# Kernel tuning notes

Hardware: AMD Instinct MI355X
Metric: run time of the kernel (lower is better)

The kernel has to match this reference:

```python
import jax, jax.numpy as jnp
import numpy as np

N_NODES = 50000
N_EDGES = 800000
HIDDEN = 128
N_LAYERS = 3
N_MASKED = 25000
N_GRAPHS = 64


def setup_inputs() -> dict:
    key = jax.random.key(0)
    ks = jax.random.split(key, 8)
    scale = 1.0 / np.sqrt(HIDDEN)
    return {
        "x": jax.random.normal(ks[0], (N_NODES, HIDDEN), dtype=jnp.float32),
        "edge_index": jax.random.randint(ks[1], (2, N_EDGES), 0, N_NODES, dtype=jnp.int64),
        "mask": jax.random.randint(ks[2], (N_MASKED,), 0, N_NODES, dtype=jnp.int64),
        "batch": jnp.sort(jax.random.randint(ks[3], (N_MASKED,), 0, N_GRAPHS, dtype=jnp.int64)),
        "conv_w": jax.random.normal(ks[4], (N_LAYERS, HIDDEN, HIDDEN), dtype=jnp.float32) * scale,
        "conv_b": jnp.zeros((N_LAYERS, HIDDEN), dtype=jnp.float32),
        "lt1_w": jax.random.normal(ks[5], (HIDDEN,), dtype=jnp.float32) * scale,
        "lt1_b": jnp.zeros((1,), dtype=jnp.float32),
    }


def reference(x, edge_index, mask, batch, conv_w, conv_b, lt1_w, lt1_b):
    n = x.shape[0]
    # GCNConv: add self-loops, symmetric normalization D^-1/2 (A+I) D^-1/2
    loops = jnp.arange(n, dtype=edge_index.dtype)
    src = jnp.concatenate([edge_index[0], loops])
    dst = jnp.concatenate([edge_index[1], loops])
    deg = jax.ops.segment_sum(jnp.ones_like(src, dtype=x.dtype), dst, num_segments=n)
    dinv = jax.lax.rsqrt(deg)  # deg >= 1 because of self-loops
    norm = (dinv[src] * dinv[dst])[:, None]  # [E+N, 1]

    h = x
    for l in range(N_LAYERS):
        hw = h @ conv_w[l]                                  # [N, H]
        agg = jax.ops.segment_sum(hw[src] * norm, dst, num_segments=n)
        h = jax.nn.elu(agg + conv_b[l])                     # dropout is identity in eval mode

    xm = h[mask]                                            # [M, H] masked-node features
    pooled = jax.ops.segment_max(xm, batch, num_segments=N_GRAPHS)  # global_max_pool
    return pooled @ lt1_w[:, None] + lt1_b                  # [G, 1]
```

## Files before the change

### kernel.cpp

```cpp
#include <hip/hip_runtime.h>
#include <math.h>

#define N_NODES  50000
#define N_EDGES  800000
#define HIDDEN   128
#define N_LAYERS 3
#define N_MASKED 25000
#define N_GRAPHS 64
#define XSLICE   6250
#define EPB      8192
#define NCHUNK   ((N_EDGES + EPB - 1) / EPB)

typedef __attribute__((ext_vector_type(8))) short bf16x8;
typedef __attribute__((ext_vector_type(4))) float f32x4;

#define GLOAD_LDS16(g, l) \
    __builtin_amdgcn_global_load_lds((const __attribute__((address_space(1))) void*)(g), \
                                     (__attribute__((address_space(3))) void*)(l), 16, 0, 0)

__device__ __forceinline__ unsigned fmap(float f) {
    unsigned u = __float_as_uint(f);
    return (u & 0x80000000u) ? ~u : (u | 0x80000000u);
}
__device__ __forceinline__ float funmap(unsigned u) {
    return __uint_as_float((u & 0x80000000u) ? (u & 0x7FFFFFFFu) : ~u);
}

__device__ __forceinline__ unsigned pack_split(float x) {
    unsigned u = __float_as_uint(x);
    unsigned hi = (u + 0x7fffu + ((u >> 16) & 1u)) >> 16;
    float rem = x - __uint_as_float(hi << 16);
    unsigned v = __float_as_uint(rem);
    unsigned lo = (v + 0x7fffu + ((v >> 16) & 1u)) >> 16;
    return hi | (lo << 16);
}

__global__ void init_kernel(unsigned* __restrict__ deg, unsigned* __restrict__ gmax,
                            const float* __restrict__ W,
                            unsigned short* __restrict__ Whi,
                            unsigned short* __restrict__ Wlo) {
    const int b = blockIdx.x;
    if (b < 196) {
        int i = b * 256 + threadIdx.x;
        if (i < N_NODES) deg[i] = 0u;
    } else if (b < 228) {
        int i = (b - 196) * 256 + threadIdx.x;
        if (i < N_GRAPHS * 128) gmax[i] = 0x007FFFFFu;
    } else {
        int idx = (b - 228) * 256 + threadIdx.x;
        if (idx < 3 * 16384) {
            int j     = idx & 7;
            int lane  = (idx >> 3) & 63;
            int ct    = (idx >> 9) & 7;
            int ks    = (idx >> 12) & 3;
            int layer = idx >> 14;
            int k = ks * 32 + (lane >> 4) * 8 + j;
            int n = ct * 16 + (lane & 15);
            unsigned p = pack_split(W[layer * 16384 + k * 128 + n]);
            Whi[idx] = (unsigned short)(p & 0xffffu);
            Wlo[idx] = (unsigned short)(p >> 16);
        }
    }
}

__global__ void xpack_kernel(const float* __restrict__ x, unsigned* __restrict__ xp, int n) {
    int i = blockIdx.x * 256 + threadIdx.x;
    if (i < n) xp[i] = pack_split(x[i]);
}

__global__ void count_deg_kernel(const int* __restrict__ dst, unsigned* __restrict__ deg) {
    const int xcd = blockIdx.x & 7;
    const int chunk = blockIdx.x >> 3;
    const int lo = xcd * XSLICE, hi = lo + XSLICE;
    const int base = chunk * EPB;
    const int end = (base + EPB < N_EDGES) ? base + EPB : N_EDGES;
    for (int e = base + threadIdx.x * 4; e < end; e += 256 * 4) {
        int4 d4 = *(const int4*)(dst + e);
        if (d4.x >= lo && d4.x < hi) atomicAdd(&deg[d4.x], 1u);
        if (d4.y >= lo && d4.y < hi) atomicAdd(&deg[d4.y], 1u);
        if (d4.z >= lo && d4.z < hi) atomicAdd(&deg[d4.z], 1u);
        if (d4.w >= lo && d4.w < hi) atomicAdd(&deg[d4.w], 1u);
    }
}

__global__ void scan_block_kernel(const unsigned* __restrict__ deg, unsigned* __restrict__ incl,
                                  unsigned* __restrict__ bsum) {
    __shared__ unsigned s[1024];
    int i = blockIdx.x * 1024 + threadIdx.x;
    unsigned v = (i < N_NODES) ? deg[i] : 0u;
    s[threadIdx.x] = v;
    __syncthreads();
    for (int off = 1; off < 1024; off <<= 1) {
        unsigned t = (threadIdx.x >= off) ? s[threadIdx.x - off] : 0u;
        __syncthreads();
        s[threadIdx.x] += t;
        __syncthreads();
    }
    if (i < N_NODES) incl[i] = s[threadIdx.x];
    if (threadIdx.x == 1023) bsum[blockIdx.x] = s[1023];
}

__global__ void scan_bsum_kernel(unsigned* __restrict__ bsum, int n) {
    int lane = threadIdx.x;
    unsigned v = (lane < n) ? bsum[lane] : 0u;
    #pragma unroll
    for (int off = 1; off < 64; off <<= 1) {
        unsigned t = __shfl_up(v, off);
        if (lane >= off) v += t;
    }
    unsigned ex = __shfl_up(v, 1);
    if (lane == 0) ex = 0u;
    if (lane < n) bsum[lane] = ex;
}

__global__ void scan_finalize_kernel(const unsigned* __restrict__ incl,
                                     const unsigned* __restrict__ bsum_ex,
                                     const unsigned* __restrict__ deg,
                                     unsigned* __restrict__ row_ptr,
                                     unsigned* __restrict__ cursor,
                                     float* __restrict__ dinv) {
    int i = blockIdx.x * blockDim.x + threadIdx.x;
    if (i <= N_NODES) {
        unsigned v = (i == 0) ? 0u : incl[i - 1] + bsum_ex[(i - 1) >> 10];
        row_ptr[i] = v;
        if (i < N_NODES) {
            cursor[(size_t)i << 4] = v;
            dinv[i] = rsqrtf((float)(deg[i] + 1u));
        }
    }
}

__global__ void fill_csr_kernel(const int* __restrict__ src, const int* __restrict__ dst,
                                unsigned* __restrict__ cursor, int* __restrict__ csr_src) {
    const int xcd = blockIdx.x & 7;
    const int chunk = blockIdx.x >> 3;
    const int lo = xcd * XSLICE, hi = lo + XSLICE;
    const int base = chunk * EPB;
    const int end = (base + EPB < N_EDGES) ? base + EPB : N_EDGES;
    for (int e = base + threadIdx.x * 4; e < end; e += 256 * 4) {
        int4 d4 = *(const int4*)(dst + e);
        int4 s4 = *(const int4*)(src + e);
        if (d4.x >= lo && d4.x < hi) csr_src[atomicAdd(&cursor[(size_t)d4.x << 4], 1u)] = s4.x;
        if (d4.y >= lo && d4.y < hi) csr_src[atomicAdd(&cursor[(size_t)d4.y << 4], 1u)] = s4.y;
        if (d4.z >= lo && d4.z < hi) csr_src[atomicAdd(&cursor[(size_t)d4.z << 4], 1u)] = s4.z;
        if (d4.w >= lo && d4.w < hi) csr_src[atomicAdd(&cursor[(size_t)d4.w << 4], 1u)] = s4.w;
    }
}

template<int MODE>
__global__ __launch_bounds__(512, 1) void mfma_gemm_kernel(const unsigned* __restrict__ Ap,
                                                           const unsigned short* __restrict__ Wh,
                                                           const unsigned short* __restrict__ Wl,
                                                           const float* __restrict__ dinv,
                                                           const float* __restrict__ bias,
                                                           const int* __restrict__ batch,
                                                           unsigned* __restrict__ gmax,
                                                           float* __restrict__ Out,
                                                           int nrows) {
    extern __shared__ char smem[];
    unsigned short* WhL = (unsigned short*)smem;
    unsigned short* WlL = (unsigned short*)(smem + 32768);
    uint4* AL4 = (uint4*)(smem + 65536);
    const int tid = threadIdx.x;
    const int lane = tid & 63;
    const int w = tid >> 6;

    #pragma unroll
    for (int i = 0; i < 4; ++i) {
        int m = tid + i * 512;
        GLOAD_LDS16((const char*)Wh + (size_t)m * 16, smem + (size_t)m * 16);
        GLOAD_LDS16((const char*)Wl + (size_t)m * 16, smem + 32768 + (size_t)m * 16);
    }

    const int ntiles = (nrows + 127) >> 7;
    const int rloc = w * 16 + (lane & 15);
    const int rx = rloc & 7;
    const int colBase = lane & 15;
    const int rgrp = lane >> 4;

    for (int t = blockIdx.x; t < ntiles; t += gridDim.x) {
        const int tileBase = t * 128;
        __syncthreads();

        #pragma unroll
        for (int i = 0; i < 8; ++i) {
            int n = tid + i * 512;
            int r = n >> 5;
            int c = n & 31;
            int grow = tileBase + r;
            if (grow > nrows - 1) grow = nrows - 1;
            GLOAD_LDS16(Ap + (size_t)grow * 128 + ((c ^ (r & 7)) << 2),
                        smem + 65536 + (size_t)n * 16);
        }
        __syncthreads();

        f32x4 acc[8];
        #pragma unroll
        for (int c = 0; c < 8; ++c) acc[c] = (f32x4){0.f, 0.f, 0.f, 0.f};

        #pragma unroll
        for (int ks = 0; ks < 4; ++ks) {
            int c0 = ks * 8 + (lane >> 4) * 2;
            uint4 a0 = AL4[rloc * 32 + (c0 ^ rx)];
            uint4 a1 = AL4[rloc * 32 + ((c0 + 1) ^ rx)];
            unsigned pv[8] = {a0.x, a0.y, a0.z, a0.w, a1.x, a1.y, a1.z, a1.w};
            bf16x8 ah, al;
            #pragma unroll
            for (int j = 0; j < 8; ++j) {
                ah[j] = (short)(pv[j] & 0xffffu);
                al[j] = (short)(pv[j] >> 16);
            }
            const unsigned short* wbh = WhL + ks * 4096 + lane * 8;
            const unsigned short* wbl = WlL + ks * 4096 + lane * 8;
            #pragma unroll
            for (int ct = 0; ct < 8; ++ct) {
                bf16x8 bh = *(const bf16x8*)(wbh + ct * 512);
                bf16x8 bl = *(const bf16x8*)(wbl + ct * 512);
                acc[ct] = __builtin_amdgcn_mfma_f32_16x16x32_bf16(ah, bh, acc[ct], 0, 0, 0);
                acc[ct] = __builtin_amdgcn_mfma_f32_16x16x32_bf16(al, bh, acc[ct], 0, 0, 0);
                acc[ct] = __builtin_amdgcn_mfma_f32_16x16x32_bf16(ah, bl, acc[ct], 0, 0, 0);
            }
        }

        #pragma unroll
        for (int r = 0; r < 4; ++r) {
            int row = tileBase + w * 16 + rgrp * 4 + r;
            if (row >= nrows) continue;
            float d = 0.f;
            int bofs = 0;
            if (MODE == 0 || MODE == 1) d = dinv[row];
            if (MODE == 2) bofs = batch[row] * 128;
            #pragma unroll
            for (int ct = 0; ct < 8; ++ct) {
                int col = ct * 16 + colBase;
                float o = acc[ct][r];
                if (MODE == 0) {
                    Out[(size_t)row * 128 + col] = o * d;
                } else {
                    o += bias[col];
                    o = o > 0.f ? o : expm1f(o);
                    if (MODE == 1) Out[(size_t)row * 128 + col] = o * d;
                    else           atomicMax(&gmax[bofs + col], fmap(o));
                }
            }
        }
    }
}

template<int GMODE>
__global__ __launch_bounds__(256) void gather_kernel(const float* __restrict__ tab,
                                                     const unsigned* __restrict__ row_ptr,
                                                     const int* __restrict__ csr_src,
                                                     const float* __restrict__ dinv,
                                                     const float* __restrict__ bias,
                                                     float* __restrict__ outf,
                                                     unsigned* __restrict__ outp,
                                                     const int* __restrict__ nodes,
                                                     int n_items) {
    int wid = (blockIdx.x * blockDim.x + threadIdx.x) >> 6;
    int w = wid >> 1;
    if (w >= n_items) return;
    const int f = ((wid & 1) << 6) | (threadIdx.x & 63);
    const int v = nodes ? nodes[w] : w;

    const unsigned s0 = row_ptr[v], e0 = row_ptr[v + 1];
    const float* __restrict__ base = tab + f;

    float acc[8];
    #pragma unroll
    for (int j = 0; j < 8; ++j) acc[j] = 0.f;
    acc[0] = base[(size_t)v << 7];

    unsigned i = s0;
    if (i + 8 <= e0) {
        int idx[8];
        #pragma unroll
        for (int j = 0; j < 8; ++j) idx[j] = csr_src[i + j];
        for (; i + 16 <= e0; i += 8) {
            int nxt[8];
            #pragma unroll
            for (int j = 0; j < 8; ++j) nxt[j] = csr_src[i + 8 + j];
            #pragma unroll
            for (int j = 0; j < 8; ++j) acc[j] += base[(size_t)idx[j] << 7];
            #pragma unroll
            for (int j = 0; j < 8; ++j) idx[j] = nxt[j];
        }
        #pragma unroll
        for (int j = 0; j < 8; ++j) acc[j] += base[(size_t)idx[j] << 7];
        i += 8;
    }
    if (i + 4 <= e0) {
        #pragma unroll
        for (int j = 0; j < 4; ++j) acc[j] += base[(size_t)csr_src[i + j] << 7];
        i += 4;
    }
    for (; i < e0; ++i) acc[0] += base[(size_t)csr_src[i] << 7];

    float dv = dinv[v];
    float sumall = ((acc[0] + acc[1]) + (acc[2] + acc[3])) +
                   ((acc[4] + acc[5]) + (acc[6] + acc[7]));
    if (GMODE == 0) {
        float o = dv * sumall + bias[f];
        o = o > 0.f ? o : expm1f(o);
        outf[((size_t)w << 7) + f] = o * dv;
    } else {
        outp[((size_t)w << 7) + f] = pack_split(dv * sumall);
    }
}

__global__ void pool_finish_kernel(const unsigned* __restrict__ gmax,
                                   const float* __restrict__ w, const float* __restrict__ b,
                                   float* __restrict__ out) {
    const int g = blockIdx.x;
    const int f = threadIdx.x;
    float val = funmap(gmax[g * 128 + f]) * w[f];
    #pragma unroll
    for (int off = 32; off > 0; off >>= 1) val += __shfl_down(val, off);
    __shared__ float ps[2];
    if ((threadIdx.x & 63) == 0) ps[threadIdx.x >> 6] = val;
    __syncthreads();
    if (threadIdx.x == 0) out[g] = ps[0] + ps[1] + b[0];
}

extern "C" void kernel_launch(void* const* d_in, const int* in_sizes, int n_in,
                              void* d_out, int out_size, void* d_ws, size_t ws_size,
                              hipStream_t stream) {
    const float* x      = (const float*)d_in[0];
    const int*   ei     = (const int*)d_in[1];
    const int*   mask   = (const int*)d_in[2];
    const int*   batch  = (const int*)d_in[3];
    const float* conv_w = (const float*)d_in[4];
    const float* conv_b = (const float*)d_in[5];
    const float* lt1_w  = (const float*)d_in[6];
    const float* lt1_b  = (const float*)d_in[7];
    float* out = (float*)d_out;

    const int* e_src = ei;
    const int* e_dst = ei + N_EDGES;

    char* ws = (char*)d_ws;
    auto carve = [&](size_t bytes) { char* p = ws; ws += (bytes + 255) & ~(size_t)255; return p; };
    unsigned* deg     = (unsigned*)carve(N_NODES * 4);
    float*    dinv    = (float*)   carve(N_NODES * 4);
    unsigned* row_ptr = (unsigned*)carve((N_NODES + 1) * 4);
    unsigned* cursor  = (unsigned*)carve((size_t)N_NODES * 64);
    unsigned* bsum    = (unsigned*)carve(64 * 4);
    unsigned* gmax    = (unsigned*)carve(N_GRAPHS * 128 * 4);
    unsigned short* wph = (unsigned short*)carve(3 * 16384 * 2);
    unsigned short* wpl = (unsigned short*)carve(3 * 16384 * 2);
    int*      csr_src = (int*)     carve((size_t)N_EDGES * 4);
    unsigned* xp      = (unsigned*)carve((size_t)N_NODES * HIDDEN * 4);
    char*     reg1    = carve((size_t)N_NODES * HIDDEN * 4);
    char*     reg2    = carve((size_t)N_NODES * HIDDEN * 4);
    unsigned* incl    = (unsigned*)csr_src;

    float*    bufB  = (float*)reg1;
    float*    bufB2 = (float*)reg1;
    float*    bufA  = (float*)reg2;
    unsigned* bufAp = (unsigned*)reg2;
    unsigned* bufCp = (unsigned*)reg2;

    const int NB_SCAN = (N_NODES + 1023) / 1024;

    init_kernel<<<420, 256, 0, stream>>>(deg, gmax, conv_w, wph, wpl);
    xpack_kernel<<<(N_NODES * HIDDEN + 255) / 256, 256, 0, stream>>>(x, xp, N_NODES * HIDDEN);
    count_deg_kernel<<<8 * NCHUNK, 256, 0, stream>>>(e_dst, deg);
    scan_block_kernel<<<NB_SCAN, 1024, 0, stream>>>(deg, incl, bsum);
    scan_bsum_kernel<<<1, 64, 0, stream>>>(bsum, NB_SCAN);
    scan_finalize_kernel<<<(N_NODES + 256) / 256, 256, 0, stream>>>(incl, bsum, deg,
                                                                    row_ptr, cursor, dinv);
    fill_csr_kernel<<<8 * NCHUNK, 256, 0, stream>>>(e_src, e_dst, cursor, csr_src);

    const size_t LDS_BYTES = 131072;
    auto gemm_grid = [](int rows) { int t = (rows + 127) / 128; return t < 256 ? t : 256; };
    auto ga_blocks = [](int items) { return (items * 2 * 64 + 255) / 256; };

    mfma_gemm_kernel<0><<<gemm_grid(N_NODES), 512, LDS_BYTES, stream>>>(
        xp, wph, wpl, dinv, nullptr, nullptr, nullptr, bufA, N_NODES);
    gather_kernel<0><<<ga_blocks(N_NODES), 256, 0, stream>>>(
        bufA, row_ptr, csr_src, dinv, conv_b, bufB, nullptr, nullptr, N_NODES);
    gather_kernel<1><<<ga_blocks(N_NODES), 256, 0, stream>>>(
        bufB, row_ptr, csr_src, dinv, nullptr, nullptr, bufAp, nullptr, N_NODES);
    mfma_gemm_kernel<1><<<gemm_grid(N_NODES), 512, LDS_BYTES, stream>>>(
        bufAp, wph + 16384, wpl + 16384, dinv, conv_b + HIDDEN, nullptr, nullptr,
        bufB2, N_NODES);
    gather_kernel<1><<<ga_blocks(N_MASKED), 256, 0, stream>>>(
        bufB2, row_ptr, csr_src, dinv, nullptr, nullptr, bufCp, mask, N_MASKED);
    mfma_gemm_kernel<2><<<gemm_grid(N_MASKED), 512, LDS_BYTES, stream>>>(
        bufCp, wph + 32768, wpl + 32768, nullptr, conv_b + 2 * HIDDEN, batch, gmax,
        nullptr, N_MASKED);

    pool_finish_kernel<<<N_GRAPHS, HIDDEN, 0, stream>>>(gmax, lt1_w, lt1_b, out);
}
```

Baseline: 362.1 us.

## Build CSR with per-group LDS histograms and cursors instead of global atomics

Degree counting now uses LDS histograms per (edge group, node slice) block and writes partial counts. The scan kernel sums them, and the finalize step turns them into per-group start offsets. The CSR fill then uses LDS cursors instead of global atomics on padded cursor slots. Deg zeroing, weight packing, gmax init and a vectorized x packing are folded into one launch, which removes kernel launches and global atomic traffic. The cost is a 32x N_NODES partial array and a 32-iteration serial loop per node in finalize. Fill parallelism also drops to 256 blocks.

```diff
diff --git a/kernel.cpp b/kernel.cpp
--- a/kernel.cpp
+++ b/kernel.cpp
@@ -8,8 +8,8 @@
 #define N_MASKED 25000
 #define N_GRAPHS 64
 #define XSLICE   6250
-#define EPB      8192
-#define NCHUNK   ((N_EDGES + EPB - 1) / EPB)
+#define NGRP     32
+#define CPG      (N_EDGES / NGRP)
 
 typedef __attribute__((ext_vector_type(8))) short bf16x8;
 typedef __attribute__((ext_vector_type(4))) float f32x4;
@@ -35,19 +35,37 @@
     return hi | (lo << 16);
 }
 
-__global__ void init_kernel(unsigned* __restrict__ deg, unsigned* __restrict__ gmax,
-                            const float* __restrict__ W,
-                            unsigned short* __restrict__ Whi,
-                            unsigned short* __restrict__ Wlo) {
+__global__ void build_kernel(const int* __restrict__ dst, unsigned* __restrict__ partial,
+                             unsigned* __restrict__ gmax, const float* __restrict__ W,
+                             unsigned short* __restrict__ Whi, unsigned short* __restrict__ Wlo,
+                             const float* __restrict__ x, unsigned* __restrict__ xp) {
     const int b = blockIdx.x;
-    if (b < 196) {
-        int i = b * 256 + threadIdx.x;
-        if (i < N_NODES) deg[i] = 0u;
-    } else if (b < 228) {
-        int i = (b - 196) * 256 + threadIdx.x;
+    const int tid = threadIdx.x;
+    if (b < 256) {
+        __shared__ unsigned hist[XSLICE];
+        const int xcd = b & 7;
+        const int g = b >> 3;
+        const int lo = xcd * XSLICE;
+        for (int i = tid; i < XSLICE; i += 256) hist[i] = 0u;
+        __syncthreads();
+        const int base = g * CPG;
+        for (int e = base + tid * 4; e + 4 <= base + CPG; e += 1024) {
+            int4 d4 = *(const int4*)(dst + e);
+            unsigned a = (unsigned)(d4.x - lo), bq = (unsigned)(d4.y - lo);
+            unsigned c = (unsigned)(d4.z - lo), d = (unsigned)(d4.w - lo);
+            if (a < XSLICE) atomicAdd(&hist[a], 1u);
+            if (bq < XSLICE) atomicAdd(&hist[bq], 1u);
+            if (c < XSLICE) atomicAdd(&hist[c], 1u);
+            if (d < XSLICE) atomicAdd(&hist[d], 1u);
+        }
+        __syncthreads();
+        for (int i = tid; i < XSLICE; i += 256)
+            partial[(size_t)g * N_NODES + lo + i] = hist[i];
+    } else if (b < 288) {
+        int i = (b - 256) * 256 + tid;
         if (i < N_GRAPHS * 128) gmax[i] = 0x007FFFFFu;
-    } else {
-        int idx = (b - 228) * 256 + threadIdx.x;
+    } else if (b < 480) {
+        int idx = (b - 288) * 256 + tid;
         if (idx < 3 * 16384) {
             int j     = idx & 7;
             int lane  = (idx >> 3) & 63;
@@ -60,34 +78,26 @@
             Whi[idx] = (unsigned short)(p & 0xffffu);
             Wlo[idx] = (unsigned short)(p >> 16);
         }
-    }
-}
-
-__global__ void xpack_kernel(const float* __restrict__ x, unsigned* __restrict__ xp, int n) {
-    int i = blockIdx.x * 256 + threadIdx.x;
-    if (i < n) xp[i] = pack_split(x[i]);
-}
-
-__global__ void count_deg_kernel(const int* __restrict__ dst, unsigned* __restrict__ deg) {
-    const int xcd = blockIdx.x & 7;
-    const int chunk = blockIdx.x >> 3;
-    const int lo = xcd * XSLICE, hi = lo + XSLICE;
-    const int base = chunk * EPB;
-    const int end = (base + EPB < N_EDGES) ? base + EPB : N_EDGES;
-    for (int e = base + threadIdx.x * 4; e < end; e += 256 * 4) {
-        int4 d4 = *(const int4*)(dst + e);
-        if (d4.x >= lo && d4.x < hi) atomicAdd(&deg[d4.x], 1u);
-        if (d4.y >= lo && d4.y < hi) atomicAdd(&deg[d4.y], 1u);
-        if (d4.z >= lo && d4.z < hi) atomicAdd(&deg[d4.z], 1u);
-        if (d4.w >= lo && d4.w < hi) atomicAdd(&deg[d4.w], 1u);
-    }
-}
-
-__global__ void scan_block_kernel(const unsigned* __restrict__ deg, unsigned* __restrict__ incl,
-                                  unsigned* __restrict__ bsum) {
+    } else {
+        int i0 = (b - 480) * 1024 + tid * 4;
+        float4 v = *(const float4*)(x + i0);
+        uint4 pk = make_uint4(pack_split(v.x), pack_split(v.y),
+                              pack_split(v.z), pack_split(v.w));
+        *(uint4*)(xp + i0) = pk;
+    }
+}
+
+__global__ void scan_block_kernel(const unsigned* __restrict__ partial,
+                                  unsigned* __restrict__ deg,
+                                  unsigned* __restrict__ incl, unsigned* __restrict__ bsum) {
     __shared__ unsigned s[1024];
     int i = blockIdx.x * 1024 + threadIdx.x;
-    unsigned v = (i < N_NODES) ? deg[i] : 0u;
+    unsigned v = 0u;
+    if (i < N_NODES) {
+        #pragma unroll 8
+        for (int g = 0; g < NGRP; ++g) v += partial[(size_t)g * N_NODES + i];
+        deg[i] = v;
+    }
     s[threadIdx.x] = v;
     __syncthreads();
     for (int off = 1; off < 1024; off <<= 1) {
@@ -117,33 +127,46 @@
                                      const unsigned* __restrict__ bsum_ex,
                                      const unsigned* __restrict__ deg,
                                      unsigned* __restrict__ row_ptr,
-                                     unsigned* __restrict__ cursor,
+                                     unsigned* __restrict__ partial,
                                      float* __restrict__ dinv) {
     int i = blockIdx.x * blockDim.x + threadIdx.x;
-    if (i <= N_NODES) {
-        unsigned v = (i == 0) ? 0u : incl[i - 1] + bsum_ex[(i - 1) >> 10];
-        row_ptr[i] = v;
-        if (i < N_NODES) {
-            cursor[(size_t)i << 4] = v;
-            dinv[i] = rsqrtf((float)(deg[i] + 1u));
+    if (i > N_NODES) return;
+    unsigned v = (i == 0) ? 0u : incl[i - 1] + bsum_ex[(i - 1) >> 10];
+    row_ptr[i] = v;
+    if (i < N_NODES) {
+        dinv[i] = rsqrtf((float)(deg[i] + 1u));
+        unsigned running = v;
+        #pragma unroll 1
+        for (int g = 0; g < NGRP; ++g) {
+            unsigned cnt = partial[(size_t)g * N_NODES + i];
+            partial[(size_t)g * N_NODES + i] = running;
+            running += cnt;
         }
     }
 }
 
 __global__ void fill_csr_kernel(const int* __restrict__ src, const int* __restrict__ dst,
-                                unsigned* __restrict__ cursor, int* __restrict__ csr_src) {
-    const int xcd = blockIdx.x & 7;
-    const int chunk = blockIdx.x >> 3;
-    const int lo = xcd * XSLICE, hi = lo + XSLICE;
-    const int base = chunk * EPB;
-    const int end = (base + EPB < N_EDGES) ? base + EPB : N_EDGES;
-    for (int e = base + threadIdx.x * 4; e < end; e += 256 * 4) {
+                                const unsigned* __restrict__ start,
+                                int* __restrict__ csr_src) {
+    __shared__ unsigned cur[XSLICE];
+    const int b = blockIdx.x;
+    const int tid = threadIdx.x;
+    const int xcd = b & 7;
+    const int g = b >> 3;
+    const int lo = xcd * XSLICE;
+    for (int i = tid; i < XSLICE; i += 256)
+        cur[i] = start[(size_t)g * N_NODES + lo + i];
+    __syncthreads();
+    const int base = g * CPG;
+    for (int e = base + tid * 4; e + 4 <= base + CPG; e += 1024) {
         int4 d4 = *(const int4*)(dst + e);
         int4 s4 = *(const int4*)(src + e);
-        if (d4.x >= lo && d4.x < hi) csr_src[atomicAdd(&cursor[(size_t)d4.x << 4], 1u)] = s4.x;
-        if (d4.y >= lo && d4.y < hi) csr_src[atomicAdd(&cursor[(size_t)d4.y << 4], 1u)] = s4.y;
-        if (d4.z >= lo && d4.z < hi) csr_src[atomicAdd(&cursor[(size_t)d4.z << 4], 1u)] = s4.z;
-        if (d4.w >= lo && d4.w < hi) csr_src[atomicAdd(&cursor[(size_t)d4.w << 4], 1u)] = s4.w;
+        unsigned a = (unsigned)(d4.x - lo), bq = (unsigned)(d4.y - lo);
+        unsigned c = (unsigned)(d4.z - lo), d = (unsigned)(d4.w - lo);
+        if (a < XSLICE) csr_src[atomicAdd(&cur[a], 1u)] = s4.x;
+        if (bq < XSLICE) csr_src[atomicAdd(&cur[bq], 1u)] = s4.y;
+        if (c < XSLICE) csr_src[atomicAdd(&cur[c], 1u)] = s4.z;
+        if (d < XSLICE) csr_src[atomicAdd(&cur[d], 1u)] = s4.w;
     }
 }
 
@@ -343,7 +366,7 @@
     unsigned* deg     = (unsigned*)carve(N_NODES * 4);
     float*    dinv    = (float*)   carve(N_NODES * 4);
     unsigned* row_ptr = (unsigned*)carve((N_NODES + 1) * 4);
-    unsigned* cursor  = (unsigned*)carve((size_t)N_NODES * 64);
+    unsigned* partial = (unsigned*)carve((size_t)NGRP * N_NODES * 4);
     unsigned* bsum    = (unsigned*)carve(64 * 4);
     unsigned* gmax    = (unsigned*)carve(N_GRAPHS * 128 * 4);
     unsigned short* wph = (unsigned short*)carve(3 * 16384 * 2);
@@ -361,15 +384,15 @@
     unsigned* bufCp = (unsigned*)reg2;
 
     const int NB_SCAN = (N_NODES + 1023) / 1024;
-
-    init_kernel<<<420, 256, 0, stream>>>(deg, gmax, conv_w, wph, wpl);
-    xpack_kernel<<<(N_NODES * HIDDEN + 255) / 256, 256, 0, stream>>>(x, xp, N_NODES * HIDDEN);
-    count_deg_kernel<<<8 * NCHUNK, 256, 0, stream>>>(e_dst, deg);
-    scan_block_kernel<<<NB_SCAN, 1024, 0, stream>>>(deg, incl, bsum);
+    const int XPACK_BLOCKS = N_NODES * HIDDEN / 1024;
+
+    build_kernel<<<480 + XPACK_BLOCKS, 256, 0, stream>>>(e_dst, partial, gmax, conv_w,
+                                                         wph, wpl, x, xp);
+    scan_block_kernel<<<NB_SCAN, 1024, 0, stream>>>(partial, deg, incl, bsum);
     scan_bsum_kernel<<<1, 64, 0, stream>>>(bsum, NB_SCAN);
     scan_finalize_kernel<<<(N_NODES + 256) / 256, 256, 0, stream>>>(incl, bsum, deg,
-                                                                    row_ptr, cursor, dinv);
-    fill_csr_kernel<<<8 * NCHUNK, 256, 0, stream>>>(e_src, e_dst, cursor, csr_src);
+                                                                    row_ptr, partial, dinv);
+    fill_csr_kernel<<<256, 256, 0, stream>>>(e_src, e_dst, partial, csr_src);
 
     const size_t LDS_BYTES = 131072;
     auto gemm_grid = [](int rows) { int t = (rows + 127) / 128; return t < 256 ? t : 256; };
```

Measured after the change: 322.3 us. 1.12x faster.
